# Optimization experiments

Hardware: AMD Instinct MI355X
Metric: run time of the kernel (lower is better)

Reference implementation:

```python
import jax, jax.numpy as jnp
import numpy as np

D_MODEL = 1024
N_HEADS = 4  # hardcoded in the torch reshape
EPS = 1e-5


def setup_inputs() -> dict:
    key = jax.random.key(0)
    ks = jax.random.split(key, 5)
    d = D_MODEL
    x = jax.random.normal(ks[0], (4, 2048, d), dtype=jnp.float32)
    scale = 1.0 / np.sqrt(d)
    qkv_w = jax.random.normal(ks[1], (3 * d, d), dtype=jnp.float32) * scale
    qkv_b = jnp.zeros((3 * d,), dtype=jnp.float32)
    wo_w = jax.random.normal(ks[2], (d, d), dtype=jnp.float32) * scale
    wo_b = jnp.zeros((d,), dtype=jnp.float32)
    gamma = jnp.ones((d,), dtype=jnp.float32)
    beta = jnp.zeros((d,), dtype=jnp.float32)
    return {"x": x, "qkv_w": qkv_w, "qkv_b": qkv_b, "wo_w": wo_w,
            "wo_b": wo_b, "gamma": gamma, "beta": beta}


def reference(x, qkv_w, qkv_b, wo_w, wo_b, gamma, beta):
    b, s, d = x.shape
    h = N_HEADS
    hd = d // h
    # QKV projection (torch Linear: x @ W.T + b)
    qkv = x @ qkv_w.T + qkv_b                      # [b, s, 3d]
    qkv = qkv.reshape(b, s, 3, h, hd)
    qkv = jnp.transpose(qkv, (2, 0, 3, 1, 4))      # [3, b, h, s, hd]
    q, k, v = qkv[0], qkv[1], qkv[2]
    scores = jnp.einsum('bhqd,bhkd->bhqk', q, k) * (hd ** -0.5)
    attn = jax.nn.softmax(scores, axis=-1)
    out = jnp.einsum('bhqk,bhkd->bhqd', attn, v)   # [b, h, s, hd]
    out = jnp.transpose(out, (0, 2, 1, 3)).reshape(b, s, d)
    y = x + (out @ wo_w.T + wo_b)
    # LayerNorm over last dim
    mu = jnp.mean(y, axis=-1, keepdims=True)
    var = jnp.var(y, axis=-1, keepdims=True)
    return (y - mu) * jax.lax.rsqrt(var + EPS) * gamma + beta
```

## Files before the change

### kernel.cpp

```cpp
#include <hip/hip_runtime.h>
#include <hip/hip_bf16.h>

#define SEQ 2048
#define DM  1024
#define NH  4
#define HD  256

typedef __attribute__((ext_vector_type(4))) float f32x4;
typedef __attribute__((ext_vector_type(16))) float f32x16;
typedef __attribute__((ext_vector_type(8))) short bf16x8;

__device__ __forceinline__ void gload16(const void* g, void* l) {
  __builtin_amdgcn_global_load_lds(
      (__attribute__((address_space(1))) void*)(unsigned long long)(g),
      (__attribute__((address_space(3))) void*)(l), 16, 0, 0);
}

__device__ __forceinline__ bf16x8 ldg8(const __hip_bfloat16* p) {
  return *reinterpret_cast<const bf16x8*>(p);
}

__device__ __forceinline__ unsigned pack2(float a, float b) {
  __hip_bfloat162 t = __float22bfloat162_rn(make_float2(a, b));
  return *reinterpret_cast<unsigned*>(&t);
}

__device__ __forceinline__ short bfbits(float x) {
  __hip_bfloat16 h = __float2bfloat16(x);
  return *reinterpret_cast<short*>(&h);
}

__global__ __launch_bounds__(256) void cvt_f32_bf16(const float* __restrict__ in,
                                                    __hip_bfloat16* __restrict__ out, int n4) {
  int i = blockIdx.x * 256 + threadIdx.x;
  if (i >= n4) return;
  float4 v = reinterpret_cast<const float4*>(in)[i];
  __hip_bfloat162* o2 = reinterpret_cast<__hip_bfloat162*>(out);
  o2[i * 2 + 0] = __float22bfloat162_rn(make_float2(v.x, v.y));
  o2[i * 2 + 1] = __float22bfloat162_rn(make_float2(v.z, v.w));
}

template <int EPI>
__global__ __launch_bounds__(256, 2) void gemm_bt(
    const __hip_bfloat16* __restrict__ A, const __hip_bfloat16* __restrict__ Bw,
    const float* __restrict__ bias, const float* __restrict__ resid,
    __hip_bfloat16* __restrict__ Cb, float* __restrict__ Cf, int M, int N, int K) {
  __shared__ __hip_bfloat16 ldsA[128 * 32];
  __shared__ __hip_bfloat16 ldsB[128 * 32];
  const int t = threadIdx.x;
  const int w = t >> 6, l = t & 63;
  const int lg = l >> 4, li = l & 15;
  const int m0 = blockIdx.y * 128, n0 = blockIdx.x * 128;
  const int wm = (w >> 1) * 64, wn = (w & 1) * 64;
  const int c1 = t + 256;
  const __hip_bfloat16* gA0 = A + (size_t)(m0 + (t >> 2)) * K + (t & 3) * 8;
  const __hip_bfloat16* gA1 = A + (size_t)(m0 + (c1 >> 2)) * K + (c1 & 3) * 8;
  const __hip_bfloat16* gB0 = Bw + (size_t)(n0 + (t >> 2)) * K + (t & 3) * 8;
  const __hip_bfloat16* gB1 = Bw + (size_t)(n0 + (c1 >> 2)) * K + (c1 & 3) * 8;
  __hip_bfloat16* lA0 = ldsA + t * 8;
  __hip_bfloat16* lA1 = ldsA + c1 * 8;
  __hip_bfloat16* lB0 = ldsB + t * 8;
  __hip_bfloat16* lB1 = ldsB + c1 * 8;
  f32x4 acc[4][4] = {};
  for (int k0 = 0; k0 < K; k0 += 32) {
    gload16(gA0 + k0, lA0);
    gload16(gA1 + k0, lA1);
    gload16(gB0 + k0, lB0);
    gload16(gB1 + k0, lB1);
    __syncthreads();
    bf16x8 af[4], bfr[4];
#pragma unroll
    for (int i = 0; i < 4; i++) af[i] = ldg8(&ldsA[(wm + i * 16 + li) * 32 + lg * 8]);
#pragma unroll
    for (int i = 0; i < 4; i++) bfr[i] = ldg8(&ldsB[(wn + i * 16 + li) * 32 + lg * 8]);
#pragma unroll
    for (int mi = 0; mi < 4; mi++)
#pragma unroll
      for (int ni = 0; ni < 4; ni++)
        acc[mi][ni] = __builtin_amdgcn_mfma_f32_16x16x32_bf16(af[mi], bfr[ni], acc[mi][ni], 0, 0, 0);
    __syncthreads();
  }
#pragma unroll
  for (int ni = 0; ni < 4; ni++) {
    const int col = n0 + wn + ni * 16 + li;
    const float bv = bias[col];
#pragma unroll
    for (int mi = 0; mi < 4; mi++) {
      const int rowb = m0 + wm + mi * 16 + lg * 4;
#pragma unroll
      for (int r = 0; r < 4; r++) {
        const size_t idx = (size_t)(rowb + r) * N + col;
        float v = acc[mi][ni][r] + bv;
        if (EPI) {
          Cf[idx] = v + resid[idx];
        } else {
          Cb[idx] = __float2bfloat16(v);
        }
      }
    }
  }
}

__global__ __launch_bounds__(256) void transpose_v(const short* __restrict__ qkv,
                                                   short* __restrict__ vt) {
  __shared__ short tile[32][36];
  const int t = threadIdx.x;
  const int bh = blockIdx.z, b = bh >> 2, h = bh & 3;
  const int s0 = blockIdx.x * 32, d0 = blockIdx.y * 32;
  const int sr = t >> 3, c4 = (t & 7) * 4;
  const short* src = qkv + (size_t)(b * SEQ + s0 + sr) * 3072 + 2048 + h * HD + d0 + c4;
  short4 vv = *reinterpret_cast<const short4*>(src);
  tile[sr][c4 + 0] = vv.x;
  tile[sr][c4 + 1] = vv.y;
  tile[sr][c4 + 2] = vv.z;
  tile[sr][c4 + 3] = vv.w;
  __syncthreads();
  short* dst = vt + (size_t)(bh * HD + d0 + sr) * SEQ + s0 + c4;
  short4 ov;
  ov.x = tile[c4 + 0][sr];
  ov.y = tile[c4 + 1][sr];
  ov.z = tile[c4 + 2][sr];
  ov.w = tile[c4 + 3][sr];
  *reinterpret_cast<short4*>(dst) = ov;
}

__global__ __launch_bounds__(512, 2) void flash_attn(const __hip_bfloat16* __restrict__ qkv,
                                                     const __hip_bfloat16* __restrict__ vt,
                                                     __hip_bfloat16* __restrict__ attno) {
  __shared__ __hip_bfloat16 ldsK[2][64 * 256];
  __shared__ __hip_bfloat16 ldsV[2][256 * 64];
  __shared__ float mlx[8][2][32];
  const int tid = threadIdx.x, w = tid >> 6, l = tid & 63;
  const int l31 = l & 31, hi = l >> 5;
  const int g = w >> 2, gt = tid & 255;
  const int bid = blockIdx.x;
  const int bh = (bid & 7) * 2 + ((bid >> 3) & 1);
  const int qt = bid >> 4;
  const int b = bh >> 2, h = bh & 3;
  const int qsub = qt * 128 + (w & 3) * 32;
  const int kvbase = g * 1024;
  bf16x8 bq[16];
  {
    const __hip_bfloat16* Qp = qkv + (size_t)(b * SEQ + qsub + l31) * 3072 + h * HD + hi * 8;
#pragma unroll
    for (int kst = 0; kst < 16; kst++) bq[kst] = ldg8(Qp + kst * 16);
  }
  const int kcd = (gt & 31) ^ ((gt >> 5) & 7);
  const __hip_bfloat16* Kg =
      qkv + (size_t)(b * SEQ + kvbase + (gt >> 5)) * 3072 + 1024 + h * HD + kcd * 8;
  const int vcd = (gt & 7) ^ ((gt >> 3) & 7);
  const __hip_bfloat16* Vg =
      vt + (size_t)bh * HD * SEQ + (size_t)(gt >> 3) * SEQ + kvbase + vcd * 8;
  __hip_bfloat16* lK = &ldsK[g][0];
  __hip_bfloat16* lV = &ldsV[g][0];

  f32x16 oacc[8] = {};
  float m_run = -1e30f, lsum = 0.f;

  for (int t = 0; t < 16; ++t) {
#pragma unroll
    for (int i = 0; i < 8; i++)
      gload16(Kg + (size_t)(t * 64 + i * 8) * 3072, lK + i * 2048 + gt * 8);
#pragma unroll
    for (int i = 0; i < 8; i++)
      gload16(Vg + (size_t)(i * 32) * SEQ + t * 64, lV + i * 2048 + gt * 8);
    __syncthreads();
#pragma unroll
    for (int t32 = 0; t32 < 2; t32++) {
      f32x16 sa = {}, sb = {};
      const int krow = t32 * 32 + l31;
      const int ksw = krow & 7;
#pragma unroll
      for (int kst = 0; kst < 8; kst++) {
        bf16x8 aka = ldg8(&lK[krow * 256 + (((4 * kst + hi) ^ ksw) << 3)]);
        bf16x8 akb = ldg8(&lK[krow * 256 + (((4 * kst + 2 + hi) ^ ksw) << 3)]);
        sa = __builtin_amdgcn_mfma_f32_32x32x16_bf16(aka, bq[2 * kst], sa, 0, 0, 0);
        sb = __builtin_amdgcn_mfma_f32_32x32x16_bf16(akb, bq[2 * kst + 1], sb, 0, 0, 0);
      }
#pragma unroll
      for (int r = 0; r < 16; r++) sa[r] = (sa[r] + sb[r]) * 0.0625f;
      float rmax = sa[0];
#pragma unroll
      for (int r = 1; r < 16; r++) rmax = fmaxf(rmax, sa[r]);
      rmax = fmaxf(rmax, __shfl_xor(rmax, 32));
      if (rmax > m_run + 8.f) {
        const float alpha = __expf(m_run - rmax);
        m_run = rmax;
        lsum *= alpha;
#pragma unroll
        for (int dt = 0; dt < 8; dt++)
#pragma unroll
          for (int r = 0; r < 16; r++) oacc[dt][r] *= alpha;
      }
      float psum = 0.f;
#pragma unroll
      for (int r = 0; r < 16; r++) {
        sa[r] = __expf(sa[r] - m_run);
        psum += sa[r];
      }
      lsum += psum + __shfl_xor(psum, 32);
#pragma unroll
      for (int s16 = 0; s16 < 2; s16++) {
        const int rb = s16 * 8;
        unsigned a0 = pack2(sa[rb + 0], sa[rb + 1]);
        unsigned a1 = pack2(sa[rb + 2], sa[rb + 3]);
        unsigned b0 = pack2(sa[rb + 4], sa[rb + 5]);
        unsigned b1 = pack2(sa[rb + 6], sa[rb + 7]);
        unsigned s0 = (unsigned)__shfl_xor((int)(hi ? a0 : b0), 32);
        unsigned s1 = (unsigned)__shfl_xor((int)(hi ? a1 : b1), 32);
        union { unsigned u[4]; bf16x8 v; } pw;
        pw.u[0] = hi ? s0 : a0;
        pw.u[1] = hi ? s1 : a1;
        pw.u[2] = hi ? b0 : s0;
        pw.u[3] = hi ? b1 : s1;
        const int vch = t32 * 4 + s16 * 2 + hi;
#pragma unroll
        for (int dt = 0; dt < 8; dt++) {
          const int drow = dt * 32 + l31;
          bf16x8 av = ldg8(&lV[drow * 64 + ((vch ^ (drow & 7)) << 3)]);
          oacc[dt] = __builtin_amdgcn_mfma_f32_32x32x16_bf16(av, pw.v, oacc[dt], 0, 0, 0);
        }
      }
    }
    __syncthreads();
  }
  if (l < 32) {
    mlx[w][0][l] = m_run;
    mlx[w][1][l] = lsum;
  }
  __syncthreads();
  {
    const float m_o = mlx[w ^ 4][0][l31];
    const float l_o = mlx[w ^ 4][1][l31];
    const float mm = fmaxf(m_run, m_o);
    const float e_s = __expf(m_run - mm), e_o = __expf(m_o - mm);
    const float wgt = e_s / (e_s * lsum + e_o * l_o);
#pragma unroll
    for (int dt = 0; dt < 8; dt++)
#pragma unroll
      for (int r = 0; r < 16; r++) oacc[dt][r] *= wgt;
  }
  const int pair = w & 3;
  float* xch = pair < 2 ? reinterpret_cast<float*>(&ldsK[0][0]) + pair * 8192
                        : reinterpret_cast<float*>(&ldsV[0][0]) + (pair - 2) * 8192;
  if (g == 0) {
#pragma unroll
    for (int dt = 0; dt < 8; dt++)
#pragma unroll
      for (int rq = 0; rq < 4; rq++) {
        const int dch = dt * 8 + 2 * rq + hi;
        f32x4 v;
#pragma unroll
        for (int i = 0; i < 4; i++) v[i] = oacc[dt][4 * rq + i];
        *reinterpret_cast<f32x4*>(&xch[l31 * 256 + ((dch ^ (l31 & 7)) << 2)]) = v;
      }
  }
  __syncthreads();
  if (g == 1) {
    const size_t rowb = (size_t)(b * SEQ + qsub + l31) * DM + h * HD;
#pragma unroll
    for (int dt = 0; dt < 8; dt++)
#pragma unroll
      for (int rq = 0; rq < 4; rq++) {
        const int dch = dt * 8 + 2 * rq + hi;
        f32x4 p = *reinterpret_cast<const f32x4*>(&xch[l31 * 256 + ((dch ^ (l31 & 7)) << 2)]);
        short4 sv;
        sv.x = bfbits(p[0] + oacc[dt][4 * rq + 0]);
        sv.y = bfbits(p[1] + oacc[dt][4 * rq + 1]);
        sv.z = bfbits(p[2] + oacc[dt][4 * rq + 2]);
        sv.w = bfbits(p[3] + oacc[dt][4 * rq + 3]);
        *reinterpret_cast<short4*>(
            reinterpret_cast<short*>(attno + rowb + dt * 32 + 8 * rq + 4 * hi)) = sv;
      }
  }
}

__global__ __launch_bounds__(256) void layernorm_k(const float* __restrict__ y,
                                                   const float* __restrict__ gamma,
                                                   const float* __restrict__ beta,
                                                   float* __restrict__ out) {
  const int w = threadIdx.x >> 6, l = threadIdx.x & 63;
  const size_t row = (size_t)blockIdx.x * 4 + w;
  const float4* yp = reinterpret_cast<const float4*>(y + row * DM);
  float4 v[4];
  float s = 0.f, s2 = 0.f;
#pragma unroll
  for (int i = 0; i < 4; i++) {
    v[i] = yp[i * 64 + l];
    s += v[i].x + v[i].y + v[i].z + v[i].w;
    s2 += v[i].x * v[i].x + v[i].y * v[i].y + v[i].z * v[i].z + v[i].w * v[i].w;
  }
#pragma unroll
  for (int off = 1; off < 64; off <<= 1) {
    s += __shfl_xor(s, off);
    s2 += __shfl_xor(s2, off);
  }
  const float mu = s * (1.f / 1024.f);
  const float rs = rsqrtf(s2 * (1.f / 1024.f) - mu * mu + 1e-5f);
  const float4* gp = reinterpret_cast<const float4*>(gamma);
  const float4* bp = reinterpret_cast<const float4*>(beta);
  float4* op = reinterpret_cast<float4*>(out + row * DM);
#pragma unroll
  for (int i = 0; i < 4; i++) {
    float4 g = gp[i * 64 + l], bb = bp[i * 64 + l];
    float4 o;
    o.x = (v[i].x - mu) * rs * g.x + bb.x;
    o.y = (v[i].y - mu) * rs * g.y + bb.y;
    o.z = (v[i].z - mu) * rs * g.z + bb.z;
    o.w = (v[i].w - mu) * rs * g.w + bb.w;
    op[i * 64 + l] = o;
  }
}

extern "C" void kernel_launch(void* const* d_in, const int* in_sizes, int n_in,
                              void* d_out, int out_size, void* d_ws, size_t ws_size,
                              hipStream_t stream) {
  const float* x     = (const float*)d_in[0];
  const float* qkv_w = (const float*)d_in[1];
  const float* qkv_b = (const float*)d_in[2];
  const float* wo_w  = (const float*)d_in[3];
  const float* wo_b  = (const float*)d_in[4];
  const float* gamma = (const float*)d_in[5];
  const float* beta  = (const float*)d_in[6];
  float* out = (float*)d_out;
  char* ws = (char*)d_ws;
  __hip_bfloat16* xbf   = (__hip_bfloat16*)(ws);
  __hip_bfloat16* qkvwb = (__hip_bfloat16*)(ws + 16777216);
  __hip_bfloat16* wowb  = (__hip_bfloat16*)(ws + 23068672);
  __hip_bfloat16* qkv   = (__hip_bfloat16*)(ws + 25165824);
  float*          yb    = (float*)(ws + 25165824);
  __hip_bfloat16* vt    = (__hip_bfloat16*)(ws + 75497472);
  __hip_bfloat16* attno = xbf;

  cvt_f32_bf16<<<8192, 256, 0, stream>>>(x, xbf, 2097152);
  cvt_f32_bf16<<<3072, 256, 0, stream>>>(qkv_w, qkvwb, 786432);
  cvt_f32_bf16<<<1024, 256, 0, stream>>>(wo_w, wowb, 262144);
  gemm_bt<0><<<dim3(24, 64), 256, 0, stream>>>(xbf, qkvwb, qkv_b, nullptr, qkv, nullptr,
                                               8192, 3072, 1024);
  transpose_v<<<dim3(64, 8, 16), 256, 0, stream>>>((const short*)qkv, (short*)vt);
  flash_attn<<<256, 512, 0, stream>>>(qkv, vt, attno);
  gemm_bt<1><<<dim3(8, 64), 256, 0, stream>>>(attno, wowb, wo_b, x, nullptr, yb,
                                              8192, 1024, 1024);
  layernorm_k<<<2048, 256, 0, stream>>>(yb, gamma, beta, out);
}
```

Baseline: 255.3 us.

## Double-buffer K/V tiles in flash attention with 32-key prefetch

Splits the per-group K/V LDS tile into two 32-key halves used as a ping-pong buffer. The loads for the next key block are issued before computing on the current one, so global-to-LDS traffic overlaps the MFMA and softmax work instead of stalling behind a barrier. This doubles the number of loop iterations and barriers and shrinks each tile, and the V swizzle is changed to fit the narrower rows. Total LDS stays the same.

```diff
diff --git a/kernel.cpp b/kernel.cpp
--- a/kernel.cpp
+++ b/kernel.cpp
@@ -127,8 +127,8 @@
 __global__ __launch_bounds__(512, 2) void flash_attn(const __hip_bfloat16* __restrict__ qkv,
                                                      const __hip_bfloat16* __restrict__ vt,
                                                      __hip_bfloat16* __restrict__ attno) {
-  __shared__ __hip_bfloat16 ldsK[2][64 * 256];
-  __shared__ __hip_bfloat16 ldsV[2][256 * 64];
+  __shared__ __hip_bfloat16 ldsK[2][2][32 * 256];
+  __shared__ __hip_bfloat16 ldsV[2][2][256 * 32];
   __shared__ float mlx[8][2][32];
   const int tid = threadIdx.x, w = tid >> 6, l = tid & 63;
   const int l31 = l & 31, hi = l >> 5;
@@ -148,78 +148,85 @@
   const int kcd = (gt & 31) ^ ((gt >> 5) & 7);
   const __hip_bfloat16* Kg =
       qkv + (size_t)(b * SEQ + kvbase + (gt >> 5)) * 3072 + 1024 + h * HD + kcd * 8;
-  const int vcd = (gt & 7) ^ ((gt >> 3) & 7);
+  const int vcd = (gt & 3) ^ ((gt >> 2) & 3);
   const __hip_bfloat16* Vg =
-      vt + (size_t)bh * HD * SEQ + (size_t)(gt >> 3) * SEQ + kvbase + vcd * 8;
-  __hip_bfloat16* lK = &ldsK[g][0];
-  __hip_bfloat16* lV = &ldsV[g][0];
+      vt + (size_t)bh * HD * SEQ + (size_t)(gt >> 2) * SEQ + kvbase + vcd * 8;
+  __hip_bfloat16* lKb[2] = {&ldsK[g][0][0], &ldsK[g][1][0]};
+  __hip_bfloat16* lVb[2] = {&ldsV[g][0][0], &ldsV[g][1][0]};
 
   f32x16 oacc[8] = {};
   float m_run = -1e30f, lsum = 0.f;
 
-  for (int t = 0; t < 16; ++t) {
-#pragma unroll
-    for (int i = 0; i < 8; i++)
-      gload16(Kg + (size_t)(t * 64 + i * 8) * 3072, lK + i * 2048 + gt * 8);
-#pragma unroll
-    for (int i = 0; i < 8; i++)
-      gload16(Vg + (size_t)(i * 32) * SEQ + t * 64, lV + i * 2048 + gt * 8);
-    __syncthreads();
-#pragma unroll
-    for (int t32 = 0; t32 < 2; t32++) {
-      f32x16 sa = {}, sb = {};
-      const int krow = t32 * 32 + l31;
-      const int ksw = krow & 7;
-#pragma unroll
-      for (int kst = 0; kst < 8; kst++) {
-        bf16x8 aka = ldg8(&lK[krow * 256 + (((4 * kst + hi) ^ ksw) << 3)]);
-        bf16x8 akb = ldg8(&lK[krow * 256 + (((4 * kst + 2 + hi) ^ ksw) << 3)]);
-        sa = __builtin_amdgcn_mfma_f32_32x32x16_bf16(aka, bq[2 * kst], sa, 0, 0, 0);
-        sb = __builtin_amdgcn_mfma_f32_32x32x16_bf16(akb, bq[2 * kst + 1], sb, 0, 0, 0);
-      }
-#pragma unroll
-      for (int r = 0; r < 16; r++) sa[r] = (sa[r] + sb[r]) * 0.0625f;
-      float rmax = sa[0];
-#pragma unroll
-      for (int r = 1; r < 16; r++) rmax = fmaxf(rmax, sa[r]);
-      rmax = fmaxf(rmax, __shfl_xor(rmax, 32));
-      if (rmax > m_run + 8.f) {
-        const float alpha = __expf(m_run - rmax);
-        m_run = rmax;
-        lsum *= alpha;
-#pragma unroll
-        for (int dt = 0; dt < 8; dt++)
-#pragma unroll
-          for (int r = 0; r < 16; r++) oacc[dt][r] *= alpha;
-      }
-      float psum = 0.f;
-#pragma unroll
-      for (int r = 0; r < 16; r++) {
-        sa[r] = __expf(sa[r] - m_run);
-        psum += sa[r];
-      }
-      lsum += psum + __shfl_xor(psum, 32);
-#pragma unroll
-      for (int s16 = 0; s16 < 2; s16++) {
-        const int rb = s16 * 8;
-        unsigned a0 = pack2(sa[rb + 0], sa[rb + 1]);
-        unsigned a1 = pack2(sa[rb + 2], sa[rb + 3]);
-        unsigned b0 = pack2(sa[rb + 4], sa[rb + 5]);
-        unsigned b1 = pack2(sa[rb + 6], sa[rb + 7]);
-        unsigned s0 = (unsigned)__shfl_xor((int)(hi ? a0 : b0), 32);
-        unsigned s1 = (unsigned)__shfl_xor((int)(hi ? a1 : b1), 32);
-        union { unsigned u[4]; bf16x8 v; } pw;
-        pw.u[0] = hi ? s0 : a0;
-        pw.u[1] = hi ? s1 : a1;
-        pw.u[2] = hi ? b0 : s0;
-        pw.u[3] = hi ? b1 : s1;
-        const int vch = t32 * 4 + s16 * 2 + hi;
-#pragma unroll
-        for (int dt = 0; dt < 8; dt++) {
-          const int drow = dt * 32 + l31;
-          bf16x8 av = ldg8(&lV[drow * 64 + ((vch ^ (drow & 7)) << 3)]);
-          oacc[dt] = __builtin_amdgcn_mfma_f32_32x32x16_bf16(av, pw.v, oacc[dt], 0, 0, 0);
-        }
+#pragma unroll
+  for (int i = 0; i < 4; i++) gload16(Kg + (size_t)(i * 8) * 3072, lKb[0] + i * 2048 + gt * 8);
+#pragma unroll
+  for (int i = 0; i < 4; i++) gload16(Vg + (size_t)(i * 64) * SEQ, lVb[0] + i * 2048 + gt * 8);
+  __syncthreads();
+
+#pragma unroll 2
+  for (int t = 0; t < 32; ++t) {
+    const int cur = t & 1;
+    if (t + 1 < 32) {
+      const int nk = (t + 1) * 32;
+#pragma unroll
+      for (int i = 0; i < 4; i++)
+        gload16(Kg + (size_t)(nk + i * 8) * 3072, lKb[cur ^ 1] + i * 2048 + gt * 8);
+#pragma unroll
+      for (int i = 0; i < 4; i++)
+        gload16(Vg + (size_t)(i * 64) * SEQ + nk, lVb[cur ^ 1] + i * 2048 + gt * 8);
+    }
+    const __hip_bfloat16* lK = lKb[cur];
+    const __hip_bfloat16* lV = lVb[cur];
+    f32x16 sa = {}, sb = {};
+    const int ksw = l31 & 7;
+#pragma unroll
+    for (int kst = 0; kst < 8; kst++) {
+      bf16x8 aka = ldg8(&lK[l31 * 256 + (((4 * kst + hi) ^ ksw) << 3)]);
+      bf16x8 akb = ldg8(&lK[l31 * 256 + (((4 * kst + 2 + hi) ^ ksw) << 3)]);
+      sa = __builtin_amdgcn_mfma_f32_32x32x16_bf16(aka, bq[2 * kst], sa, 0, 0, 0);
+      sb = __builtin_amdgcn_mfma_f32_32x32x16_bf16(akb, bq[2 * kst + 1], sb, 0, 0, 0);
+    }
+#pragma unroll
+    for (int r = 0; r < 16; r++) sa[r] = (sa[r] + sb[r]) * 0.0625f;
+    float rmax = sa[0];
+#pragma unroll
+    for (int r = 1; r < 16; r++) rmax = fmaxf(rmax, sa[r]);
+    rmax = fmaxf(rmax, __shfl_xor(rmax, 32));
+    if (rmax > m_run + 8.f) {
+      const float alpha = __expf(m_run - rmax);
+      m_run = rmax;
+      lsum *= alpha;
+#pragma unroll
+      for (int dt = 0; dt < 8; dt++)
+#pragma unroll
+        for (int r = 0; r < 16; r++) oacc[dt][r] *= alpha;
+    }
+    float psum = 0.f;
+#pragma unroll
+    for (int r = 0; r < 16; r++) {
+      sa[r] = __expf(sa[r] - m_run);
+      psum += sa[r];
+    }
+    lsum += psum + __shfl_xor(psum, 32);
+#pragma unroll
+    for (int ks = 0; ks < 2; ks++) {
+      const int rb = ks * 8;
+      unsigned a0 = pack2(sa[rb + 0], sa[rb + 1]);
+      unsigned a1 = pack2(sa[rb + 2], sa[rb + 3]);
+      unsigned b0 = pack2(sa[rb + 4], sa[rb + 5]);
+      unsigned b1 = pack2(sa[rb + 6], sa[rb + 7]);
+      unsigned s0 = (unsigned)__shfl_xor((int)(hi ? a0 : b0), 32);
+      unsigned s1 = (unsigned)__shfl_xor((int)(hi ? a1 : b1), 32);
+      union { unsigned u[4]; bf16x8 v; } pw;
+      pw.u[0] = hi ? s0 : a0;
+      pw.u[1] = hi ? s1 : a1;
+      pw.u[2] = hi ? b0 : s0;
+      pw.u[3] = hi ? b1 : s1;
+#pragma unroll
+      for (int dt = 0; dt < 8; dt++) {
+        const int drow = dt * 32 + l31;
+        bf16x8 av = ldg8(&lV[drow * 32 + (((ks * 2 + hi) ^ (drow & 3)) << 3)]);
+        oacc[dt] = __builtin_amdgcn_mfma_f32_32x32x16_bf16(av, pw.v, oacc[dt], 0, 0, 0);
       }
     }
     __syncthreads();
@@ -241,8 +248,8 @@
       for (int r = 0; r < 16; r++) oacc[dt][r] *= wgt;
   }
   const int pair = w & 3;
-  float* xch = pair < 2 ? reinterpret_cast<float*>(&ldsK[0][0]) + pair * 8192
-                        : reinterpret_cast<float*>(&ldsV[0][0]) + (pair - 2) * 8192;
+  float* xch = pair < 2 ? reinterpret_cast<float*>(&ldsK[0][0][0]) + pair * 8192
+                        : reinterpret_cast<float*>(&ldsV[0][0][0]) + (pair - 2) * 8192;
   if (g == 0) {
 #pragma unroll
     for (int dt = 0; dt < 8; dt++)
```

Result: slower. 261.3 us (+2.4%).
